# Optimization experiments

Measured on AMD Instinct MI355X. Metric: run time of the kernel, lower is better.

## Reference

```python
import jax, jax.numpy as jnp
import numpy as np

B, L, S, E, H = 2, 2048, 2048, 1024, 16
D = E // H


def setup_inputs() -> dict:
    key = jax.random.key(0)
    ks = jax.random.split(key, 16)
    p = 0.02  # small init scale for weights
    return {
        "a": jax.random.normal(ks[0], (B, L, E), jnp.float32),
        "b": jax.random.normal(ks[1], (B, S, E), jnp.float32),
        "Wa_qk": jax.random.normal(ks[2], (E, E), jnp.float32) * p,
        "ba_qk": jax.random.normal(ks[3], (E,), jnp.float32) * p,
        "Wa_v": jax.random.normal(ks[4], (E, E), jnp.float32) * p,
        "ba_v": jax.random.normal(ks[5], (E,), jnp.float32) * p,
        "Wb_qk": jax.random.normal(ks[6], (E, E), jnp.float32) * p,
        "bb_qk": jax.random.normal(ks[7], (E,), jnp.float32) * p,
        "Wb_v": jax.random.normal(ks[8], (E, E), jnp.float32) * p,
        "bb_v": jax.random.normal(ks[9], (E,), jnp.float32) * p,
        "Wa_o": jax.random.normal(ks[10], (E, E), jnp.float32) * p,
        "ba_o": jax.random.normal(ks[11], (E,), jnp.float32) * p,
        "Wb_o": jax.random.normal(ks[12], (E, E), jnp.float32) * p,
        "bb_o": jax.random.normal(ks[13], (E,), jnp.float32) * p,
    }


def _heads(x, n, W, bias):
    # x: [B, N, E] -> projected and split to [B, H, N, D]
    y = x @ W + bias
    return y.reshape(B, n, H, D).transpose(0, 2, 1, 3)


def reference(a, b, Wa_qk, ba_qk, Wa_v, ba_v, Wb_qk, bb_qk, Wb_v, bb_v,
              Wa_o, ba_o, Wb_o, bb_o):
    aq = _heads(a, L, Wa_qk, ba_qk)   # [B,H,L,D]
    av = _heads(a, L, Wa_v, ba_v)     # [B,H,L,D]
    bq = _heads(b, S, Wb_qk, bb_qk)   # [B,H,S,D]
    bv = _heads(b, S, Wb_v, bb_v)     # [B,H,S,D]

    scale = 1.0 / jnp.sqrt(jnp.float32(D))
    # Shared score matrix [B,H,L,S]
    scores = jnp.einsum('bhld,bhsd->bhls', aq, bq) * scale
    # Dual softmax: row-wise (over S) and column-wise (over L)
    wa = jax.nn.softmax(scores, axis=-1)                    # [B,H,L,S]
    wb = jax.nn.softmax(scores, axis=-2).transpose(0, 1, 3, 2)  # [B,H,S,L]

    a_ctx = jnp.einsum('bhls,bhsd->bhld', wa, bv)  # [B,H,L,D]
    b_ctx = jnp.einsum('bhsl,bhld->bhsd', wb, av)  # [B,H,S,D]

    a_out = a_ctx.transpose(0, 2, 1, 3).reshape(B, L, E) @ Wa_o + ba_o
    b_out = b_ctx.transpose(0, 2, 1, 3).reshape(B, S, E) @ Wb_o + bb_o
    return (a_out, b_out)
```

## Files before the change

### kernel.cpp

```cpp
#include <hip/hip_runtime.h>
#include <hip/hip_bf16.h>
#include <stdint.h>

typedef unsigned short u16;
typedef unsigned int u32;
typedef __attribute__((ext_vector_type(8))) short bf16x8;
typedef __attribute__((ext_vector_type(4))) float f32x4;

typedef __attribute__((address_space(3))) void lds_void;
typedef const __attribute__((address_space(1))) void gbl_void;

#define SIDE 4194304u
#define BHSTR 131072u

static __device__ __forceinline__ u16 f2bf(float f) {
  union { __hip_bfloat16 b; u16 u; } cv;
  cv.b = __float2bfloat16(f);
  return cv.u;
}
static __device__ __forceinline__ float bf2f(u16 u) {
  union { __hip_bfloat16 b; u16 u; } cv;
  cv.u = u;
  return __bfloat162float(cv.b);
}

__global__ __launch_bounds__(256) void k_cvt_in(const float* __restrict__ a,
                                                const float* __restrict__ b,
                                                u16* __restrict__ dst) {
  int z = blockIdx.y;
  const float* src = z ? b : a;
  size_t i = ((size_t)blockIdx.x * 256 + threadIdx.x) * 8;
  float4 x0 = *(const float4*)(src + i);
  float4 x1 = *(const float4*)(src + i + 4);
  u16 t[8] = {f2bf(x0.x), f2bf(x0.y), f2bf(x0.z), f2bf(x0.w),
              f2bf(x1.x), f2bf(x1.y), f2bf(x1.z), f2bf(x1.w)};
  *(uint4*)(dst + (size_t)z * SIDE + i) = *(uint4*)t;
}

__global__ __launch_bounds__(256) void k_cvt_bias(
    const float* s0, const float* s1, const float* s2, const float* s3,
    const float* s4, const float* s5, u16* __restrict__ dst) {
  const float* srcs[6] = {s0, s1, s2, s3, s4, s5};
  int z = blockIdx.y;
  int i = blockIdx.x * 256 + threadIdx.x;
  float sc = (z == 0) ? 0.18033688011112042f : 1.0f;
  dst[z * 1024 + i] = f2bf(srcs[z][i] * sc);
}

__global__ __launch_bounds__(256) void k_transpose_w(
    const float* a0, const float* a1, const float* a2, const float* a3,
    const float* a4, const float* a5,
    u16* d0, u16* d1, u16* d2, u16* d3, u16* d4, u16* d5) {
  __shared__ u16 tile[64][72];
  const float* srcs[6] = {a0, a1, a2, a3, a4, a5};
  u16* dsts[6] = {d0, d1, d2, d3, d4, d5};
  int z = blockIdx.z;
  float sc = (z == 0) ? 0.18033688011112042f : 1.0f;
  const float* src = srcs[z] + (size_t)(blockIdx.y * 64) * 1024 + blockIdx.x * 64;
  int t = threadIdx.x;
  int row = t >> 2, c4 = t & 3;
#pragma unroll
  for (int p = 0; p < 2; ++p) {
    int col = c4 * 8 + p * 32;
    const float* sf = src + (size_t)row * 1024 + col;
    float4 x0 = *(const float4*)sf;
    float4 x1 = *(const float4*)(sf + 4);
    u16 tmp[8] = {f2bf(x0.x * sc), f2bf(x0.y * sc), f2bf(x0.z * sc), f2bf(x0.w * sc),
                  f2bf(x1.x * sc), f2bf(x1.y * sc), f2bf(x1.z * sc), f2bf(x1.w * sc)};
    *(uint4*)(&tile[row][col]) = *(uint4*)tmp;
  }
  __syncthreads();
  u16* dst = dsts[z] + (size_t)(blockIdx.x * 64) * 1024 + blockIdx.y * 64;
#pragma unroll
  for (int p = 0; p < 2; ++p) {
    int col = c4 * 8 + p * 32;
    u16 tmp[8];
#pragma unroll
    for (int i = 0; i < 8; ++i) tmp[i] = tile[col + i][row];
    *(uint4*)(dst + (size_t)row * 1024 + col) = *(uint4*)tmp;
  }
}

__global__ __launch_bounds__(256) void k_gemm_qkv(
    const u16* __restrict__ Aall, const u16* __restrict__ WtA,
    const u16* __restrict__ WtB, const u16* __restrict__ bias,
    u16* __restrict__ qkbuf, u16* __restrict__ vbuf) {
  __shared__ u16 Sh[8192];
  u16* As = Sh;
  u16* Bs = Sh + 4096;
  int tid = threadIdx.x;
  int wave = tid >> 6, lane = tid & 63;
  int quad = lane >> 4, lrow = lane & 15;
  int wr = wave >> 1, wc = wave & 1;
  int z = blockIdx.z;
  int m0 = blockIdx.y * 128, n0 = blockIdx.x * 128;
  const u16* A = Aall + (size_t)z * SIDE;
  const u16* Wt = z ? WtB : WtA;
  const u16* bi = bias + (size_t)z * 2048;

  f32x4 acc[4][4] = {};
  int srow = 32 * wave + (lane >> 2);
  int scol = (lane & 3) * 8;
  const u16* gA = A + (size_t)(m0 + srow) * 1024 + scol;
  const u16* gB = Wt + (size_t)(n0 + srow) * 1024 + scol;
  u16* lA = &As[(32 * wave) * 32];
  u16* lB = &Bs[(32 * wave) * 32];

  for (int k0 = 0; k0 < 1024; k0 += 32) {
    __syncthreads();
#pragma unroll
    for (int j = 0; j < 2; ++j) {
      __builtin_amdgcn_global_load_lds((gbl_void*)(gA + (size_t)(16 * j) * 1024 + k0),
                                       (lds_void*)(lA + 16 * j * 32), 16, 0, 0);
      __builtin_amdgcn_global_load_lds((gbl_void*)(gB + (size_t)(16 * j) * 1024 + k0),
                                       (lds_void*)(lB + 16 * j * 32), 16, 0, 0);
    }
    __syncthreads();
    bf16x8 af[4], bfr[4];
#pragma unroll
    for (int i = 0; i < 4; ++i)
      af[i] = *(const bf16x8*)&As[(64 * wr + 16 * i + lrow) * 32 + 8 * quad];
#pragma unroll
    for (int j = 0; j < 4; ++j)
      bfr[j] = *(const bf16x8*)&Bs[(64 * wc + 16 * j + lrow) * 32 + 8 * quad];
#pragma unroll
    for (int i = 0; i < 4; ++i)
#pragma unroll
      for (int j = 0; j < 4; ++j)
        acc[i][j] = __builtin_amdgcn_mfma_f32_16x16x32_bf16(af[i], bfr[j], acc[i][j], 0, 0, 0);
  }

  float bv[4];
#pragma unroll
  for (int j = 0; j < 4; ++j) bv[j] = bf2f(bi[n0 + 64 * wc + 16 * j + lrow]);

  int x = blockIdx.x;
  bool isv = (x >= 8);
  int h = (isv ? 2 * (x - 8) : 2 * x) + wc;
  u16* dst = (isv ? vbuf : qkbuf) + (size_t)z * SIDE;
  u16* lw = Sh + wave * 1216;

  __syncthreads();
#pragma unroll
  for (int i = 0; i < 4; ++i) {
#pragma unroll
    for (int j = 0; j < 4; ++j)
#pragma unroll
      for (int r = 0; r < 4; ++r)
        lw[(4 * quad + r) * 76 + 16 * j + lrow] = f2bf(acc[i][j][r] + bv[j]);
    asm volatile("s_waitcnt lgkmcnt(0)" ::: "memory");
    int row = lane >> 2, cg = (lane & 3) * 16;
    int rg = m0 + 64 * wr + 16 * i + row;
    int bb = rg >> 11, rl = rg & 2047;
    u16* dr = dst + (size_t)(bb * 16 + h) * BHSTR + (size_t)rl * 64 + cg;
    uint2 w0 = *(const uint2*)&lw[row * 76 + cg];
    uint2 w1 = *(const uint2*)&lw[row * 76 + cg + 4];
    uint2 w2 = *(const uint2*)&lw[row * 76 + cg + 8];
    uint2 w3 = *(const uint2*)&lw[row * 76 + cg + 12];
    uint4 o0 = {w0.x, w0.y, w1.x, w1.y};
    uint4 o1 = {w2.x, w2.y, w3.x, w3.y};
    *(uint4*)dr = o0;
    *(uint4*)(dr + 8) = o1;
    asm volatile("s_waitcnt lgkmcnt(0)" ::: "memory");
  }
}

__global__ __launch_bounds__(256) void k_transpose_v(const u16* __restrict__ v,
                                                     u16* __restrict__ vt) {
  __shared__ u16 tile[64][72];
  int sbh = blockIdx.y;
  int n0 = blockIdx.x * 64;
  const u16* src = v + (size_t)sbh * BHSTR + (size_t)n0 * 64;
  u16* dst = vt + (size_t)sbh * BHSTR + n0;
  int t = threadIdx.x;
  int row = t >> 2, c4 = t & 3;
#pragma unroll
  for (int p = 0; p < 2; ++p) {
    int col = c4 * 8 + p * 32;
    uint4 q = *(const uint4*)(src + (size_t)row * 64 + col);
    *(uint4*)(&tile[row][col]) = q;
  }
  __syncthreads();
#pragma unroll
  for (int p = 0; p < 2; ++p) {
    int col = c4 * 8 + p * 32;
    u16 tmp[8];
#pragma unroll
    for (int i = 0; i < 8; ++i) tmp[i] = tile[col + i][row];
    *(uint4*)(dst + (size_t)row * 2048 + col) = *(uint4*)tmp;
  }
}

__global__ __launch_bounds__(256, 4) void k_attn(
    const u16* __restrict__ qk, const u16* __restrict__ vt,
    u16* __restrict__ ctx) {
  __shared__ u16 Ks[2 * 2048];
  __shared__ u16 Vs[2 * 2048];
  __shared__ u16 Ps[4 * 1024];
  int tid = threadIdx.x;
  int wave = tid >> 6, lane = tid & 63;
  int quad = lane >> 4, lrow = lane & 15;
  int z = blockIdx.z, bh = blockIdx.x;
  int l0 = blockIdx.y * 128;
  const u16* Qb = qk + (size_t)z * SIDE + (size_t)bh * BHSTR + (size_t)l0 * 64;
  const u16* Kb = qk + (size_t)(1 - z) * SIDE + (size_t)bh * BHSTR;
  const u16* Vtb = vt + (size_t)(1 - z) * SIDE + (size_t)bh * BHSTR;

  bf16x8 qf[2][2];
#pragma unroll
  for (int rt = 0; rt < 2; ++rt) {
    int lq = 32 * wave + 16 * rt + lrow;
    qf[rt][0] = *(const bf16x8*)&Qb[(size_t)lq * 64 + 8 * quad];
    qf[rt][1] = *(const bf16x8*)&Qb[(size_t)lq * 64 + 32 + 8 * quad];
  }

  int gk = wave * 64 + lane;
  int krow = gk >> 3, kc = gk & 7;
  int vrow = gk >> 2, vc = gk & 3;
  const u16* kSrc = Kb + (size_t)krow * 64 + ((kc ^ (krow & 7)) * 8);
  const u16* vSrc = Vtb + (size_t)vrow * 2048 + ((vc ^ (vrow & 3)) * 8);
  u16* kDst = Ks + wave * 512;
  u16* vDst = Vs + wave * 512;

  bf16x8 ones;
  {
    short o = 0x3F80;
#pragma unroll
    for (int i = 0; i < 8; ++i) ones[i] = o;
  }

  f32x4 cacc[2][4] = {};
  f32x4 asum[2] = {};
  int ew = 2 * (lrow & 3);
  u16* Pw = Ps + wave * 1024;
  int kof0 = (quad ^ (lrow & 7)) * 8;
  int kof1 = ((quad + 4) ^ (lrow & 7)) * 8;
  int vof = (quad ^ (lrow & 3)) * 8;
  int prof = ((2 * quad) ^ ew) * 4;

  __builtin_amdgcn_global_load_lds((gbl_void*)kSrc, (lds_void*)kDst, 16, 0, 0);
  __builtin_amdgcn_global_load_lds((gbl_void*)vSrc, (lds_void*)vDst, 16, 0, 0);

#define ATT_BODY(BUF, IT)                                                      \
  {                                                                            \
    const u16* KsC = Ks + (BUF)*2048;                                          \
    const u16* VsC = Vs + (BUF)*2048;                                          \
    _Pragma("unroll") for (int j = 0; j < 2; ++j) {                            \
      int kr = 16 * j + lrow;                                                  \
      bf16x8 kf0 = *(const bf16x8*)&KsC[kr * 64 + kof0];                       \
      bf16x8 kf1 = *(const bf16x8*)&KsC[kr * 64 + kof1];                       \
      _Pragma("unroll") for (int rt = 0; rt < 2; ++rt) {                       \
        f32x4 s = {};                                                          \
        s = __builtin_amdgcn_mfma_f32_16x16x32_bf16(kf0, qf[rt][0], s, 0, 0, 0); \
        s = __builtin_amdgcn_mfma_f32_16x16x32_bf16(kf1, qf[rt][1], s, 0, 0, 0); \
        float e0 = exp2f(s[0]), e1 = exp2f(s[1]);                              \
        float e2 = exp2f(s[2]), e3 = exp2f(s[3]);                              \
        uint2 pk;                                                              \
        pk.x = ((u32)f2bf(e1) << 16) | (u32)f2bf(e0);                          \
        pk.y = ((u32)f2bf(e3) << 16) | (u32)f2bf(e2);                          \
        *(uint2*)&Pw[(16 * rt + lrow) * 32 + (((4 * j + quad) ^ ew) * 4)] = pk; \
      }                                                                        \
    }                                                                          \
    asm volatile("s_waitcnt lgkmcnt(0)" ::: "memory");                         \
    bf16x8 pf0 = *(const bf16x8*)&Pw[lrow * 32 + prof];                        \
    bf16x8 pf1 = *(const bf16x8*)&Pw[(16 + lrow) * 32 + prof];                 \
    _Pragma("unroll") for (int jd = 0; jd < 4; ++jd) {                         \
      int vr = 16 * jd + lrow;                                                 \
      bf16x8 vf = *(const bf16x8*)&VsC[vr * 32 + vof];                         \
      cacc[0][jd] = __builtin_amdgcn_mfma_f32_16x16x32_bf16(pf0, vf, cacc[0][jd], 0, 0, 0); \
      cacc[1][jd] = __builtin_amdgcn_mfma_f32_16x16x32_bf16(pf1, vf, cacc[1][jd], 0, 0, 0); \
    }                                                                          \
    asum[0] = __builtin_amdgcn_mfma_f32_16x16x32_bf16(pf0, ones, asum[0], 0, 0, 0); \
    asum[1] = __builtin_amdgcn_mfma_f32_16x16x32_bf16(pf1, ones, asum[1], 0, 0, 0); \
  }

  for (int it2 = 0; it2 < 32; ++it2) {
    int it = it2 * 2;
    __syncthreads();
    __builtin_amdgcn_global_load_lds((gbl_void*)(kSrc + (size_t)(it + 1) * 2048),
                                     (lds_void*)(kDst + 2048), 16, 0, 0);
    __builtin_amdgcn_global_load_lds((gbl_void*)(vSrc + (it + 1) * 32),
                                     (lds_void*)(vDst + 2048), 16, 0, 0);
    ATT_BODY(0, it)
    __syncthreads();
    if (it2 < 31) {
      __builtin_amdgcn_global_load_lds((gbl_void*)(kSrc + (size_t)(it + 2) * 2048),
                                       (lds_void*)kDst, 16, 0, 0);
      __builtin_amdgcn_global_load_lds((gbl_void*)(vSrc + (it + 2) * 32),
                                       (lds_void*)vDst, 16, 0, 0);
    }
    ATT_BODY(1, it + 1)
  }
#undef ATT_BODY

  int bb = bh >> 4, h = bh & 15;
  u16* Ob = ctx + (size_t)z * SIDE + (size_t)(bb * 2048 + l0) * 1024 + h * 64;
#pragma unroll
  for (int rt = 0; rt < 2; ++rt) {
#pragma unroll
    for (int r = 0; r < 4; ++r) {
      float rinv = 1.0f / asum[rt][r];
      int l = 32 * wave + 16 * rt + 4 * quad + r;
#pragma unroll
      for (int j = 0; j < 4; ++j)
        Ob[(size_t)l * 1024 + 16 * j + lrow] = f2bf(cacc[rt][j][r] * rinv);
    }
  }
}

__global__ __launch_bounds__(256) void k_gemm_o(
    const u16* __restrict__ ctx, const u16* __restrict__ WtO,
    const u16* __restrict__ bias, float* __restrict__ out) {
  __shared__ u16 As[128 * 32];
  __shared__ u16 Bs[128 * 32];
  int tid = threadIdx.x;
  int wave = tid >> 6, lane = tid & 63;
  int quad = lane >> 4, lrow = lane & 15;
  int wr = wave >> 1, wc = wave & 1;
  int z = blockIdx.z;
  int m0 = blockIdx.y * 128, n0 = blockIdx.x * 128;
  const u16* A = ctx + (size_t)z * SIDE;
  const u16* Wt = WtO + (size_t)z * 1048576;
  const u16* bi = bias + (size_t)z * 1024;
  float* C = out + (size_t)z * SIDE;

  f32x4 acc[4][4] = {};
  int srow = 32 * wave + (lane >> 2);
  int scol = (lane & 3) * 8;
  const u16* gA = A + (size_t)(m0 + srow) * 1024 + scol;
  const u16* gB = Wt + (size_t)(n0 + srow) * 1024 + scol;
  u16* lA = &As[(32 * wave) * 32];
  u16* lB = &Bs[(32 * wave) * 32];

  for (int k0 = 0; k0 < 1024; k0 += 32) {
    __syncthreads();
#pragma unroll
    for (int j = 0; j < 2; ++j) {
      __builtin_amdgcn_global_load_lds((gbl_void*)(gA + (size_t)(16 * j) * 1024 + k0),
                                       (lds_void*)(lA + 16 * j * 32), 16, 0, 0);
      __builtin_amdgcn_global_load_lds((gbl_void*)(gB + (size_t)(16 * j) * 1024 + k0),
                                       (lds_void*)(lB + 16 * j * 32), 16, 0, 0);
    }
    __syncthreads();
    bf16x8 af[4], bfr[4];
#pragma unroll
    for (int i = 0; i < 4; ++i)
      af[i] = *(const bf16x8*)&As[(64 * wr + 16 * i + lrow) * 32 + 8 * quad];
#pragma unroll
    for (int j = 0; j < 4; ++j)
      bfr[j] = *(const bf16x8*)&Bs[(64 * wc + 16 * j + lrow) * 32 + 8 * quad];
#pragma unroll
    for (int i = 0; i < 4; ++i)
#pragma unroll
      for (int j = 0; j < 4; ++j)
        acc[i][j] = __builtin_amdgcn_mfma_f32_16x16x32_bf16(af[i], bfr[j], acc[i][j], 0, 0, 0);
  }

  float bv[4];
#pragma unroll
  for (int j = 0; j < 4; ++j) bv[j] = bf2f(bi[n0 + 64 * wc + 16 * j + lrow]);
#pragma unroll
  for (int i = 0; i < 4; ++i) {
    int row = m0 + 64 * wr + 16 * i + 4 * quad;
#pragma unroll
    for (int j = 0; j < 4; ++j) {
      int col = n0 + 64 * wc + 16 * j + lrow;
#pragma unroll
      for (int r = 0; r < 4; ++r)
        C[(size_t)(row + r) * 1024 + col] = acc[i][j][r] + bv[j];
    }
  }
}

extern "C" void kernel_launch(void* const* d_in, const int* in_sizes, int n_in,
                              void* d_out, int out_size, void* d_ws, size_t ws_size,
                              hipStream_t stream) {
  (void)in_sizes; (void)n_in; (void)out_size; (void)ws_size;
  const size_t M1 = 1048576u;
  u16* ws = (u16*)d_ws;
  u16* wtA   = ws;
  u16* wtB   = ws + 2 * M1;
  u16* wtO   = ws + 4 * M1;
  u16* biasQ = ws + 6 * M1;
  u16* biasO = ws + 6 * M1 + 4096;
  u16* ab    = ws + 7 * M1;
  u16* vt    = ab;
  u16* qkbuf = ws + 15 * M1;
  u16* vbuf  = ws + 23 * M1;
  u16* ctx   = vbuf;

  dim3 blk(256);
  k_cvt_in<<<dim3(2048, 2), blk, 0, stream>>>((const float*)d_in[0],
                                              (const float*)d_in[1], ab);
  k_cvt_bias<<<dim3(4, 6), blk, 0, stream>>>(
      (const float*)d_in[3], (const float*)d_in[5], (const float*)d_in[7],
      (const float*)d_in[9], (const float*)d_in[11], (const float*)d_in[13], biasQ);
  k_transpose_w<<<dim3(16, 16, 6), blk, 0, stream>>>(
      (const float*)d_in[2], (const float*)d_in[4], (const float*)d_in[6],
      (const float*)d_in[8], (const float*)d_in[10], (const float*)d_in[12],
      wtA, wtA + M1, wtB, wtB + M1, wtO, wtO + M1);
  k_gemm_qkv<<<dim3(16, 32, 2), blk, 0, stream>>>(ab, wtA, wtB, biasQ, qkbuf, vbuf);
  k_transpose_v<<<dim3(32, 64), blk, 0, stream>>>(vbuf, vt);
  k_attn<<<dim3(32, 16, 2), blk, 0, stream>>>(qkbuf, vt, ctx);
  k_gemm_o<<<dim3(8, 32, 2), blk, 0, stream>>>(ctx, wtO, biasO, (float*)d_out);
}
```

Measured before the change: 322.0 us.

## Keep attention probabilities in registers via permlane16 swap and double tile size

After: 319.5 us. About the same (-0.8%).

```diff
diff --git a/kernel.cpp b/kernel.cpp
--- a/kernel.cpp
+++ b/kernel.cpp
@@ -22,6 +22,17 @@
   union { __hip_bfloat16 b; u16 u; } cv;
   cv.u = u;
   return __bfloat162float(cv.b);
+}
+
+static __device__ __forceinline__ void pl16swap(u32& a, u32& b) {
+#if __has_builtin(__builtin_amdgcn_permlane16_swap)
+  typedef __attribute__((ext_vector_type(2))) unsigned int u32x2;
+  u32x2 r = __builtin_amdgcn_permlane16_swap(a, b, 0, 0);
+  a = r[0];
+  b = r[1];
+#else
+  asm volatile("v_permlane16_swap_b32 %0, %1" : "+v"(a), "+v"(b));
+#endif
 }
 
 __global__ __launch_bounds__(256) void k_cvt_in(const float* __restrict__ a,
@@ -194,9 +205,8 @@
 __global__ __launch_bounds__(256, 4) void k_attn(
     const u16* __restrict__ qk, const u16* __restrict__ vt,
     u16* __restrict__ ctx) {
-  __shared__ u16 Ks[2 * 2048];
-  __shared__ u16 Vs[2 * 2048];
-  __shared__ u16 Ps[4 * 1024];
+  __shared__ u16 Ks[2 * 4096];
+  __shared__ u16 Vs[2 * 4096];
   int tid = threadIdx.x;
   int wave = tid >> 6, lane = tid & 63;
   int quad = lane >> 4, lrow = lane & 15;
@@ -214,13 +224,16 @@
     qf[rt][1] = *(const bf16x8*)&Qb[(size_t)lq * 64 + 32 + 8 * quad];
   }
 
-  int gk = wave * 64 + lane;
-  int krow = gk >> 3, kc = gk & 7;
-  int vrow = gk >> 2, vc = gk & 3;
-  const u16* kSrc = Kb + (size_t)krow * 64 + ((kc ^ (krow & 7)) * 8);
-  const u16* vSrc = Vtb + (size_t)vrow * 2048 + ((vc ^ (vrow & 3)) * 8);
-  u16* kDst = Ks + wave * 512;
-  u16* vDst = Vs + wave * 512;
+  int r0 = tid >> 3, c0 = tid & 7;
+  int r1 = (256 + tid) >> 3;
+  const u16* kS0 = Kb + (size_t)r0 * 64 + ((c0 ^ (r0 & 7)) * 8);
+  const u16* kS1 = Kb + (size_t)r1 * 64 + ((c0 ^ (r1 & 7)) * 8);
+  const u16* vS0 = Vtb + (size_t)r0 * 2048 + ((c0 ^ (r0 & 7)) * 8);
+  const u16* vS1 = Vtb + (size_t)r1 * 2048 + ((c0 ^ (r1 & 7)) * 8);
+  u16* kD0 = Ks + (wave * 64) * 8;
+  u16* kD1 = Ks + (256 + wave * 64) * 8;
+  u16* vD0 = Vs + (wave * 64) * 8;
+  u16* vD1 = Vs + (256 + wave * 64) * 8;
 
   bf16x8 ones;
   {
@@ -231,67 +244,81 @@
 
   f32x4 cacc[2][4] = {};
   f32x4 asum[2] = {};
-  int ew = 2 * (lrow & 3);
-  u16* Pw = Ps + wave * 1024;
-  int kof0 = (quad ^ (lrow & 7)) * 8;
-  int kof1 = ((quad + 4) ^ (lrow & 7)) * 8;
-  int vof = (quad ^ (lrow & 3)) * 8;
-  int prof = ((2 * quad) ^ ew) * 4;
-
-  __builtin_amdgcn_global_load_lds((gbl_void*)kSrc, (lds_void*)kDst, 16, 0, 0);
-  __builtin_amdgcn_global_load_lds((gbl_void*)vSrc, (lds_void*)vDst, 16, 0, 0);
-
-#define ATT_BODY(BUF, IT)                                                      \
-  {                                                                            \
-    const u16* KsC = Ks + (BUF)*2048;                                          \
-    const u16* VsC = Vs + (BUF)*2048;                                          \
-    _Pragma("unroll") for (int j = 0; j < 2; ++j) {                            \
-      int kr = 16 * j + lrow;                                                  \
-      bf16x8 kf0 = *(const bf16x8*)&KsC[kr * 64 + kof0];                       \
-      bf16x8 kf1 = *(const bf16x8*)&KsC[kr * 64 + kof1];                       \
-      _Pragma("unroll") for (int rt = 0; rt < 2; ++rt) {                       \
-        f32x4 s = {};                                                          \
+  int gsq = 2 * (quad & 1) + (quad >> 1);
+
+#define STAGE(BUFOFF, IT)                                                        \
+  __builtin_amdgcn_global_load_lds((gbl_void*)(kS0 + (size_t)(IT)*4096),         \
+                                   (lds_void*)(kD0 + (BUFOFF)), 16, 0, 0);       \
+  __builtin_amdgcn_global_load_lds((gbl_void*)(kS1 + (size_t)(IT)*4096),         \
+                                   (lds_void*)(kD1 + (BUFOFF)), 16, 0, 0);       \
+  __builtin_amdgcn_global_load_lds((gbl_void*)(vS0 + (size_t)(IT)*64),           \
+                                   (lds_void*)(vD0 + (BUFOFF)), 16, 0, 0);       \
+  __builtin_amdgcn_global_load_lds((gbl_void*)(vS1 + (size_t)(IT)*64),           \
+                                   (lds_void*)(vD1 + (BUFOFF)), 16, 0, 0);
+
+#define ATT_BODY(BUFOFF)                                                         \
+  {                                                                              \
+    const u16* KsC = Ks + (BUFOFF);                                              \
+    const u16* VsC = Vs + (BUFOFF);                                              \
+    u32 X[2][4], Y[2][4];                                                        \
+    _Pragma("unroll") for (int j = 0; j < 4; ++j) {                              \
+      int kr = 16 * j + lrow;                                                    \
+      bf16x8 kf0 = *(const bf16x8*)&KsC[(kr * 8 + (quad ^ (kr & 7))) * 8];       \
+      bf16x8 kf1 = *(const bf16x8*)&KsC[(kr * 8 + ((quad + 4) ^ (kr & 7))) * 8]; \
+      _Pragma("unroll") for (int rt = 0; rt < 2; ++rt) {                         \
+        f32x4 s = {};                                                            \
         s = __builtin_amdgcn_mfma_f32_16x16x32_bf16(kf0, qf[rt][0], s, 0, 0, 0); \
         s = __builtin_amdgcn_mfma_f32_16x16x32_bf16(kf1, qf[rt][1], s, 0, 0, 0); \
-        float e0 = exp2f(s[0]), e1 = exp2f(s[1]);                              \
-        float e2 = exp2f(s[2]), e3 = exp2f(s[3]);                              \
-        uint2 pk;                                                              \
-        pk.x = ((u32)f2bf(e1) << 16) | (u32)f2bf(e0);                          \
-        pk.y = ((u32)f2bf(e3) << 16) | (u32)f2bf(e2);                          \
-        *(uint2*)&Pw[(16 * rt + lrow) * 32 + (((4 * j + quad) ^ ew) * 4)] = pk; \
-      }                                                                        \
-    }                                                                          \
-    asm volatile("s_waitcnt lgkmcnt(0)" ::: "memory");                         \
-    bf16x8 pf0 = *(const bf16x8*)&Pw[lrow * 32 + prof];                        \
-    bf16x8 pf1 = *(const bf16x8*)&Pw[(16 + lrow) * 32 + prof];                 \
-    _Pragma("unroll") for (int jd = 0; jd < 4; ++jd) {                         \
-      int vr = 16 * jd + lrow;                                                 \
-      bf16x8 vf = *(const bf16x8*)&VsC[vr * 32 + vof];                         \
-      cacc[0][jd] = __builtin_amdgcn_mfma_f32_16x16x32_bf16(pf0, vf, cacc[0][jd], 0, 0, 0); \
-      cacc[1][jd] = __builtin_amdgcn_mfma_f32_16x16x32_bf16(pf1, vf, cacc[1][jd], 0, 0, 0); \
-    }                                                                          \
-    asum[0] = __builtin_amdgcn_mfma_f32_16x16x32_bf16(pf0, ones, asum[0], 0, 0, 0); \
-    asum[1] = __builtin_amdgcn_mfma_f32_16x16x32_bf16(pf1, ones, asum[1], 0, 0, 0); \
-  }
-
-  for (int it2 = 0; it2 < 32; ++it2) {
-    int it = it2 * 2;
-    __syncthreads();
-    __builtin_amdgcn_global_load_lds((gbl_void*)(kSrc + (size_t)(it + 1) * 2048),
-                                     (lds_void*)(kDst + 2048), 16, 0, 0);
-    __builtin_amdgcn_global_load_lds((gbl_void*)(vSrc + (it + 1) * 32),
-                                     (lds_void*)(vDst + 2048), 16, 0, 0);
-    ATT_BODY(0, it)
-    __syncthreads();
-    if (it2 < 31) {
-      __builtin_amdgcn_global_load_lds((gbl_void*)(kSrc + (size_t)(it + 2) * 2048),
-                                       (lds_void*)kDst, 16, 0, 0);
-      __builtin_amdgcn_global_load_lds((gbl_void*)(vSrc + (it + 2) * 32),
-                                       (lds_void*)vDst, 16, 0, 0);
+        float e0 = exp2f(s[0]), e1 = exp2f(s[1]);                                \
+        float e2 = exp2f(s[2]), e3 = exp2f(s[3]);                                \
+        X[rt][j] = ((u32)f2bf(e1) << 16) | (u32)f2bf(e0);                        \
+        Y[rt][j] = ((u32)f2bf(e3) << 16) | (u32)f2bf(e2);                        \
+      }                                                                          \
+    }                                                                            \
+    bf16x8 pf[2][2];                                                             \
+    _Pragma("unroll") for (int rt = 0; rt < 2; ++rt) {                           \
+      pl16swap(X[rt][0], X[rt][1]);                                              \
+      pl16swap(Y[rt][0], Y[rt][1]);                                              \
+      pl16swap(X[rt][2], X[rt][3]);                                              \
+      pl16swap(Y[rt][2], Y[rt][3]);                                              \
+      union { u32 d[4]; bf16x8 v; } u0, u1;                                      \
+      u0.d[0] = X[rt][0]; u0.d[1] = Y[rt][0];                                    \
+      u0.d[2] = X[rt][1]; u0.d[3] = Y[rt][1];                                    \
+      u1.d[0] = X[rt][2]; u1.d[1] = Y[rt][2];                                    \
+      u1.d[2] = X[rt][3]; u1.d[3] = Y[rt][3];                                    \
+      pf[rt][0] = u0.v;                                                          \
+      pf[rt][1] = u1.v;                                                          \
+    }                                                                            \
+    _Pragma("unroll") for (int jd = 0; jd < 4; ++jd) {                           \
+      int vr = 16 * jd + lrow;                                                   \
+      bf16x8 vf0 = *(const bf16x8*)&VsC[(vr * 8 + (gsq ^ (vr & 7))) * 8];        \
+      bf16x8 vf1 = *(const bf16x8*)&VsC[(vr * 8 + ((gsq | 4) ^ (vr & 7))) * 8];  \
+      _Pragma("unroll") for (int rt = 0; rt < 2; ++rt) {                         \
+        cacc[rt][jd] = __builtin_amdgcn_mfma_f32_16x16x32_bf16(pf[rt][0], vf0, cacc[rt][jd], 0, 0, 0); \
+        cacc[rt][jd] = __builtin_amdgcn_mfma_f32_16x16x32_bf16(pf[rt][1], vf1, cacc[rt][jd], 0, 0, 0); \
+      }                                                                          \
+    }                                                                            \
+    _Pragma("unroll") for (int rt = 0; rt < 2; ++rt) {                           \
+      asum[rt] = __builtin_amdgcn_mfma_f32_16x16x32_bf16(pf[rt][0], ones, asum[rt], 0, 0, 0); \
+      asum[rt] = __builtin_amdgcn_mfma_f32_16x16x32_bf16(pf[rt][1], ones, asum[rt], 0, 0, 0); \
+    }                                                                            \
+  }
+
+  STAGE(0, 0)
+
+  for (int it2 = 0; it2 < 16; ++it2) {
+    int it = 2 * it2;
+    __syncthreads();
+    STAGE(4096, it + 1)
+    ATT_BODY(0)
+    __syncthreads();
+    if (it2 < 15) {
+      STAGE(0, it + 2)
     }
-    ATT_BODY(1, it + 1)
+    ATT_BODY(4096)
   }
 #undef ATT_BODY
+#undef STAGE
 
   int bb = bh >> 4, h = bh & 15;
   u16* Ob = ctx + (size_t)z * SIDE + (size_t)(bb * 2048 + l0) * 1024 + h * 64;
```
